# Kernel tuning notes

Measured on AMD Instinct MI355X. Metric: run time of the kernel, lower is better.

## Reference

```python
import jax, jax.numpy as jnp
import numpy as np
import math

D = 256; NH = 8; NG = 64; META = 6

def _linear(x, w, b):
    return x @ w.T + b

def setup_inputs():
    key = jax.random.key(0)
    ks = jax.random.split(key, 12)
    B, T, TG = 32, 4096, 1024
    def rn(k, shape, s=0.02):
        return jax.random.normal(k, shape, dtype=jnp.float32) * s
    q = jax.random.normal(ks[0], (1, NG, D), dtype=jnp.float32)
    q = q / jnp.clip(jnp.linalg.norm(q, axis=-1, keepdims=True), 1e-6)
    # fibonacci unit sphere anchor, scaled by 0.4
    idx = jnp.arange(NG, dtype=jnp.float32)
    golden = (1.0 + math.sqrt(5.0)) / 2.0
    theta = 2.0 * math.pi * idx / golden
    z = jnp.clip(1.0 - (2.0 * idx + 1.0) / NG, -1.0 + 1e-6, 1.0 - 1e-6)
    r = jnp.sqrt(jnp.clip(1.0 - z * z, 0.0))
    pts = jnp.stack([r * jnp.cos(theta), r * jnp.sin(theta), z], axis=-1)
    pts = pts / jnp.clip(jnp.linalg.norm(pts, axis=-1, keepdims=True), 1e-6)
    p0 = (pts * 0.4)[None]
    ph_b2 = jnp.array([0.0] * 6 + [-2.0] * 4, dtype=jnp.float32)
    return dict(
        local_feat=jax.random.normal(ks[1], (B, D, T), dtype=jnp.float32),
        global_feat=jax.random.normal(ks[2], (B, D, TG), dtype=jnp.float32),
        meta=jax.random.uniform(ks[3], (B, META), dtype=jnp.float32),
        queries=q, p0_anchor=p0,
        in_proj_w=rn(ks[4], (3 * D, D)), in_proj_b=jnp.zeros((3 * D,), jnp.float32),
        out_proj_w=rn(ks[5], (D, D)), out_proj_b=jnp.zeros((D,), jnp.float32),
        ln_g=jnp.ones((D,), jnp.float32), ln_b=jnp.zeros((D,), jnp.float32),
        meta_w=rn(ks[6], (D, META)), meta_b=jnp.zeros((D,), jnp.float32),
        temporal_w=rn(ks[7], (D, D)), temporal_b=jnp.zeros((D,), jnp.float32),
        shift_w=rn(ks[8], (3, D)), shift_b=jnp.zeros((3,), jnp.float32),
        ph_w1=rn(ks[9], (D // 2, D)), ph_b1=jnp.zeros((D // 2,), jnp.float32),
        ph_w2=rn(ks[10], (10, D // 2)), ph_b2=ph_b2,
        wave_delay_scale=jnp.float32(0.1),
        envelope_bias=jnp.float32(0.5),
    )

def reference(local_feat, global_feat, meta, queries, p0_anchor, in_proj_w, in_proj_b,
              out_proj_w, out_proj_b, ln_g, ln_b, meta_w, meta_b, temporal_w, temporal_b,
              shift_w, shift_b, ph_w1, ph_b1, ph_w2, ph_b2, wave_delay_scale, envelope_bias):
    B, _, T = local_feat.shape
    DH = D // NH
    kv = jnp.transpose(global_feat, (0, 2, 1))                        # [B,TG,D]
    q = jnp.broadcast_to(queries, (B, NG, D))
    wq, wk, wv = in_proj_w[:D], in_proj_w[D:2 * D], in_proj_w[2 * D:]
    bq, bk, bv = in_proj_b[:D], in_proj_b[D:2 * D], in_proj_b[2 * D:]
    qh = _linear(q, wq, bq).reshape(B, NG, NH, DH)
    kh = _linear(kv, wk, bk).reshape(B, -1, NH, DH)
    vh = _linear(kv, wv, bv).reshape(B, -1, NH, DH)
    attn = jax.nn.softmax(jnp.einsum('bqhd,bkhd->bhqk', qh, kh) / math.sqrt(DH), axis=-1)
    ctx = jnp.einsum('bhqk,bkhd->bqhd', attn, vh).reshape(B, NG, D)
    x = q + _linear(ctx, out_proj_w, out_proj_b)
    mu = x.mean(-1, keepdims=True)
    var = ((x - mu) ** 2).mean(-1, keepdims=True)
    q_static = (x - mu) / jnp.sqrt(var + 1e-5) * ln_g + ln_b
    q_static = q_static + jax.nn.gelu(_linear(meta, meta_w, meta_b), approximate=False)[:, None, :]
    params = _linear(jax.nn.gelu(_linear(q_static, ph_w1, ph_b1), approximate=False), ph_w2, ph_b2)
    p0_delta = jnp.tanh(params[..., 0:3]) * 0.2
    heart_shift = jnp.tanh(_linear(global_feat.mean(-1), shift_w, shift_b)) * 0.3
    p_pos = p0_anchor + p0_delta + heart_shift[:, None, :]            # [B,NG,3]
    dnorm = jnp.clip(jnp.linalg.norm(params[..., 3:6], axis=-1, keepdims=True), 1e-6)
    dipole_dir = params[..., 3:6] / dnorm
    volume_xyz = jax.nn.sigmoid(params[..., 6:9]) * 0.5 + 0.001
    amplitude = jax.nn.sigmoid(params[..., 9]) + 1e-4                 # [B,NG]
    tw = _linear(q_static, temporal_w, temporal_b)                    # [B,NG,D]
    temporal_logits = jnp.einsum('bnc,bct->bnt', tw, local_feat) / math.sqrt(D)
    idx_sa = jnp.argmax(amplitude, axis=1)                            # [B]
    p_sa = jnp.take_along_axis(p_pos, idx_sa[:, None, None], axis=1)  # [B,1,3]
    dist = jnp.linalg.norm(p_pos - p_sa, axis=-1)                     # [B,NG]
    delay = jnp.clip(jax.nn.softplus(wave_delay_scale) * dist, 0.0, 0.1)
    base_x = jnp.linspace(-1.0, 1.0, T)
    grid_x = base_x[None, None, :] - delay[..., None]                 # [B,NG,T]
    # grid_sample(bilinear, zeros, align_corners=True): grid_y hits rows exactly,
    # so it reduces to 1D linear interp along time with zero padding.
    x_pix = (grid_x + 1.0) * 0.5 * (T - 1)
    x0 = jnp.floor(x_pix).astype(jnp.int32)
    x1 = x0 + 1
    w1 = x_pix - x0.astype(x_pix.dtype)
    w0 = 1.0 - w1
    def samp(xi):
        g = jnp.take_along_axis(temporal_logits, jnp.clip(xi, 0, T - 1), axis=-1)
        return g * ((xi >= 0) & (xi <= T - 1)).astype(g.dtype)
    shifted = w0 * samp(x0) + w1 * samp(x1)
    envelope_t = jax.nn.sigmoid(shifted + envelope_bias)              # [B,NG,T]
    return amplitude, p_pos, dipole_dir, volume_xyz, envelope_t
```

## Files before the change

### kernel.cpp

```cpp
#include <hip/hip_runtime.h>
#include <hip/hip_bf16.h>
#include <math.h>

typedef __hip_bfloat16 bf16;
typedef short s16x8 __attribute__((ext_vector_type(8)));
typedef float f32x4 __attribute__((ext_vector_type(4)));

#define NDIM 256
#define NTG 1024
#define NT 4096

__device__ __forceinline__ float gelu_exact(float x) {
    return 0.5f * x * (1.0f + erff(x * 0.70710678118654752440f));
}
__device__ __forceinline__ float sigmoidf_(float x) {
    return 1.0f / (1.0f + __expf(-x));
}
__device__ __forceinline__ short f2bf_s(float x) {
    union { bf16 h; short s; } cv;
    cv.h = __float2bfloat16(x);
    return cv.s;
}
__device__ __forceinline__ float bf2f(short s) {
    union { bf16 h; short s; } cv;
    cv.s = s;
    return __bfloat162float(cv.h);
}

__global__ __launch_bounds__(256) void k_prep(
        const float* __restrict__ ipw, const float* __restrict__ opw,
        const float* __restrict__ twm, const float* __restrict__ pw1,
        const float* __restrict__ queries, const float* __restrict__ ipb,
        float* __restrict__ opwT, float* __restrict__ twT, float* __restrict__ pw1T,
        bf16* __restrict__ wkvK, bf16* __restrict__ wkvV,
        float* __restrict__ qh, float* __restrict__ gmean) {
    int blk = blockIdx.x, tid = threadIdx.x;
    if (blk < 384) {
        int id = blk * 256 + tid;
        if (id < 65536) {
            int k = id >> 8, c = id & 255;
            opwT[id] = opw[c * 256 + k];
            twT[id]  = twm[c * 256 + k];
        } else {
            int id2 = id - 65536;
            int k = id2 >> 7, m = id2 & 127;
            pw1T[id2] = pw1[m * 256 + k];
        }
    } else if (blk < 640) {
        int id = (blk - 384) * 256 + tid;
        wkvK[id] = __float2bfloat16(ipw[65536 + id]);
        wkvV[id] = __float2bfloat16(ipw[131072 + id]);
    } else if (blk < 704) {
        __shared__ float qrow[256];
        int n = blk - 640, c = tid;
        qrow[c] = queries[n * 256 + c];
        __syncthreads();
        float s = ipb[c];
        const float* wr = ipw + c * 256;
        for (int k = 0; k < 256; ++k) s += qrow[k] * wr[k];
        qh[n * 256 + c] = s;
    } else {
        gmean[(blk - 704) * 256 + tid] = 0.f;
    }
}

__global__ __launch_bounds__(256) void k_gft(const float* __restrict__ gf,
                                             bf16* __restrict__ gfT,
                                             float* __restrict__ gmean) {
    __shared__ float tile[64][65];
    int tid = threadIdx.x;
    int t0 = blockIdx.x * 64, c0 = blockIdx.y * 64, b = blockIdx.z;
    int tt = tid & 63, ci = tid >> 6;
    #pragma unroll
    for (int r = 0; r < 16; ++r) {
        int cl = ci * 16 + r;
        tile[cl][tt] = gf[((size_t)(b * 256 + c0 + cl)) * NTG + t0 + tt];
    }
    __syncthreads();
    int cc = tid & 63, ti = tid >> 6;
    #pragma unroll
    for (int r = 0; r < 16; ++r) {
        int tl = ti * 16 + r;
        gfT[((size_t)(b * 1024 + t0 + tl)) * 256 + c0 + cc] =
            __float2bfloat16(tile[cc][tl]);
    }
    float ps = 0.f;
    #pragma unroll
    for (int r = 0; r < 16; ++r) ps += tile[cc][ti * 16 + r];
    atomicAdd(&gmean[b * 256 + c0 + cc], ps * (1.0f / 1024.0f));
}

__global__ void k_metahs(const float* __restrict__ meta, const float* __restrict__ mw,
                         const float* __restrict__ mb, const float* __restrict__ gmean,
                         const float* __restrict__ sw, const float* __restrict__ sb,
                         float* __restrict__ metag, float* __restrict__ hshift) {
    int b = blockIdx.x, c = threadIdx.x;
    float s = mb[c];
    #pragma unroll
    for (int j = 0; j < 6; ++j) s += meta[b * 6 + j] * mw[c * 6 + j];
    metag[b * 256 + c] = gelu_exact(s);
    if (c < 3) {
        float t = sb[c];
        const float* gm = gmean + b * 256;
        for (int k = 0; k < 256; ++k) t += gm[k] * sw[c * 256 + k];
        hshift[b * 4 + c] = tanhf(t) * 0.3f;
    }
}

__global__ __launch_bounds__(256) void k_kv(
        const short* __restrict__ gfT, const short* __restrict__ wkvK,
        const short* __restrict__ wkvV, const float* __restrict__ ipb,
        short* __restrict__ kvh, short* __restrict__ vTg) {
    int tid = threadIdx.x;
    int w = tid >> 6, lane = tid & 63, lm = lane & 15, quad = lane >> 4;
    int t0 = blockIdx.x * 128 + w * 32;
    int sel = blockIdx.y >> 2;
    int n0 = (blockIdx.y & 3) * 64;
    int b = blockIdx.z;
    if (sel == 0) {
        f32x4 acc[4][2];
        #pragma unroll
        for (int ni = 0; ni < 4; ++ni)
            #pragma unroll
            for (int mt = 0; mt < 2; ++mt) acc[ni][mt] = (f32x4)(0.0f);
        #pragma unroll
        for (int ks = 0; ks < 8; ++ks) {
            int c = ks * 32 + quad * 8;
            s16x8 bg[2];
            #pragma unroll
            for (int mt = 0; mt < 2; ++mt)
                bg[mt] = *(const s16x8*)&gfT[((size_t)(b * 1024 + t0 + mt * 16 + lm)) * 256 + c];
            #pragma unroll
            for (int ni = 0; ni < 4; ++ni) {
                s16x8 aw = *(const s16x8*)&wkvK[(n0 + ni * 16 + lm) * 256 + c];
                #pragma unroll
                for (int mt = 0; mt < 2; ++mt)
                    acc[ni][mt] = __builtin_amdgcn_mfma_f32_16x16x32_bf16(aw, bg[mt], acc[ni][mt], 0, 0, 0);
            }
        }
        #pragma unroll
        for (int ni = 0; ni < 4; ++ni) {
            int nb4 = n0 + ni * 16 + quad * 4;
            float4 bias = *(const float4*)&ipb[256 + nb4];
            #pragma unroll
            for (int mt = 0; mt < 2; ++mt) {
                int t = t0 + mt * 16 + lm;
                ushort4 o;
                o.x = (unsigned short)f2bf_s(acc[ni][mt][0] + bias.x);
                o.y = (unsigned short)f2bf_s(acc[ni][mt][1] + bias.y);
                o.z = (unsigned short)f2bf_s(acc[ni][mt][2] + bias.z);
                o.w = (unsigned short)f2bf_s(acc[ni][mt][3] + bias.w);
                *(ushort4*)&kvh[((size_t)(b * 1024 + t)) * 256 + nb4] = o;
            }
        }
    } else {
        f32x4 acc[2][4];
        #pragma unroll
        for (int mt = 0; mt < 2; ++mt)
            #pragma unroll
            for (int ni = 0; ni < 4; ++ni) acc[mt][ni] = (f32x4)(0.0f);
        #pragma unroll
        for (int ks = 0; ks < 8; ++ks) {
            int c = ks * 32 + quad * 8;
            s16x8 ag[2];
            #pragma unroll
            for (int mt = 0; mt < 2; ++mt)
                ag[mt] = *(const s16x8*)&gfT[((size_t)(b * 1024 + t0 + mt * 16 + lm)) * 256 + c];
            #pragma unroll
            for (int ni = 0; ni < 4; ++ni) {
                s16x8 bw = *(const s16x8*)&wkvV[(n0 + ni * 16 + lm) * 256 + c];
                #pragma unroll
                for (int mt = 0; mt < 2; ++mt)
                    acc[mt][ni] = __builtin_amdgcn_mfma_f32_16x16x32_bf16(ag[mt], bw, acc[mt][ni], 0, 0, 0);
            }
        }
        #pragma unroll
        for (int ni = 0; ni < 4; ++ni) {
            int nv = n0 + ni * 16 + lm;
            float bias = ipb[512 + nv];
            #pragma unroll
            for (int mt = 0; mt < 2; ++mt) {
                int t4 = t0 + mt * 16 + quad * 4;
                ushort4 o;
                o.x = (unsigned short)f2bf_s(acc[mt][ni][0] + bias);
                o.y = (unsigned short)f2bf_s(acc[mt][ni][1] + bias);
                o.z = (unsigned short)f2bf_s(acc[mt][ni][2] + bias);
                o.w = (unsigned short)f2bf_s(acc[mt][ni][3] + bias);
                *(ushort4*)&vTg[((size_t)(b * 256 + nv)) * 1024 + t4] = o;
            }
        }
    }
}

__global__ __launch_bounds__(256) void k_attn(
        const short* __restrict__ kvh, const short* __restrict__ vTg,
        const float* __restrict__ qh,
        float* __restrict__ o_half, float* __restrict__ l_half) {
    __shared__ short pT[4][64 * 40];
    __shared__ float obuf[4][64 * 36];
    __shared__ float lbuf[4 * 64];
    int tid = threadIdx.x;
    int w = tid >> 6, lane = tid & 63, lm = lane & 15, quad = lane >> 4;
    int half = blockIdx.x, h = blockIdx.y, b = blockIdx.z;
    s16x8 aq[4];
    #pragma unroll
    for (int mt = 0; mt < 4; ++mt) {
        const float* qp = qh + (mt * 16 + lm) * 256 + h * 32 + quad * 8;
        #pragma unroll
        for (int j = 0; j < 8; ++j) aq[mt][j] = f2bf_s(qp[j]);
    }
    f32x4 acco[2][4];
    #pragma unroll
    for (int dt = 0; dt < 2; ++dt)
        #pragma unroll
        for (int qt = 0; qt < 4; ++qt) acco[dt][qt] = (f32x4)(0.0f);
    float lp[4][4];
    #pragma unroll
    for (int mt = 0; mt < 4; ++mt)
        #pragma unroll
        for (int r = 0; r < 4; ++r) lp[mt][r] = 0.f;
    const float scale = 0.17677669529663687f;
    int kb = half * 512 + w * 128;
    for (int ch = 0; ch < 4; ++ch) {
        int n0 = kb + ch * 32;
        #pragma unroll
        for (int nt = 0; nt < 2; ++nt) {
            int key = n0 + nt * 16 + lm;
            s16x8 bk = *(const s16x8*)&kvh[((size_t)(b * 1024 + key)) * 256 + h * 32 + quad * 8];
            f32x4 zero = {0.f, 0.f, 0.f, 0.f};
            #pragma unroll
            for (int mt = 0; mt < 4; ++mt) {
                f32x4 S = __builtin_amdgcn_mfma_f32_16x16x32_bf16(aq[mt], bk, zero, 0, 0, 0);
                #pragma unroll
                for (int r = 0; r < 4; ++r) {
                    float e = __expf(S[r] * scale);
                    lp[mt][r] += e;
                    pT[w][(mt * 16 + quad * 4 + r) * 40 + nt * 16 + lm] = f2bf_s(e);
                }
            }
        }
        s16x8 av[2], bp[4];
        #pragma unroll
        for (int dt = 0; dt < 2; ++dt)
            av[dt] = *(const s16x8*)&vTg[((size_t)(b * 256 + h * 32 + dt * 16 + lm)) * 1024 + n0 + quad * 8];
        #pragma unroll
        for (int qt = 0; qt < 4; ++qt)
            bp[qt] = *(const s16x8*)&pT[w][(qt * 16 + lm) * 40 + quad * 8];
        #pragma unroll
        for (int dt = 0; dt < 2; ++dt)
            #pragma unroll
            for (int qt = 0; qt < 4; ++qt)
                acco[dt][qt] = __builtin_amdgcn_mfma_f32_16x16x32_bf16(av[dt], bp[qt], acco[dt][qt], 0, 0, 0);
    }
    #pragma unroll
    for (int mt = 0; mt < 4; ++mt)
        #pragma unroll
        for (int r = 0; r < 4; ++r) {
            float v = lp[mt][r];
            v += __shfl_xor(v, 1); v += __shfl_xor(v, 2);
            v += __shfl_xor(v, 4); v += __shfl_xor(v, 8);
            lp[mt][r] = v;
        }
    #pragma unroll
    for (int dt = 0; dt < 2; ++dt)
        #pragma unroll
        for (int qt = 0; qt < 4; ++qt) {
            int q = qt * 16 + lm;
            float4 t;
            t.x = acco[dt][qt][0]; t.y = acco[dt][qt][1];
            t.z = acco[dt][qt][2]; t.w = acco[dt][qt][3];
            *(float4*)&obuf[w][q * 36 + dt * 16 + quad * 4] = t;
        }
    if (lm == 0) {
        #pragma unroll
        for (int mt = 0; mt < 4; ++mt)
            #pragma unroll
            for (int r = 0; r < 4; ++r)
                lbuf[w * 64 + mt * 16 + quad * 4 + r] = lp[mt][r];
    }
    __syncthreads();
    int q = tid & 63, dg = tid >> 6;
    int blk = (b * 8 + h) * 2 + half;
    float l = lbuf[q] + lbuf[64 + q] + lbuf[128 + q] + lbuf[192 + q];
    float o[8];
    #pragma unroll
    for (int j = 0; j < 8; ++j) o[j] = 0.f;
    #pragma unroll
    for (int w2 = 0; w2 < 4; ++w2) {
        const float* src = &obuf[w2][q * 36 + dg * 8];
        #pragma unroll
        for (int j = 0; j < 8; ++j) o[j] += src[j];
    }
    float* dst = &o_half[(((size_t)blk * 64) + q) * 32 + dg * 8];
    #pragma unroll
    for (int j = 0; j < 8; ++j) dst[j] = o[j];
    if (dg == 0) l_half[blk * 64 + q] = l;
}

__global__ __launch_bounds__(256) void k_post(
        const float* __restrict__ o_half, const float* __restrict__ l_half,
        const float* __restrict__ queries,
        const float* __restrict__ opwT, const float* __restrict__ opb,
        const float* __restrict__ lng, const float* __restrict__ lnb,
        const float* __restrict__ metag, const float* __restrict__ hshift,
        const float* __restrict__ twT, const float* __restrict__ tbv,
        const float* __restrict__ pw1T, const float* __restrict__ pb1,
        const float* __restrict__ pw2, const float* __restrict__ pb2,
        const float* __restrict__ p0a,
        bf16* __restrict__ twbf, float* __restrict__ out_amp,
        float* __restrict__ out_ppos, float* __restrict__ out_dip,
        float* __restrict__ out_vol) {
    __shared__ float cs[8][256];
    __shared__ float xs[8][256];
    __shared__ float qs[8][256];
    __shared__ float h1[8][128];
    __shared__ float ps[8][10];
    int tid = threadIdx.x;
    int n0 = blockIdx.x * 8, b = blockIdx.y;
    {
        int h = tid >> 5, d = tid & 31;
        int blk0 = (b * 8 + h) * 2;
        #pragma unroll
        for (int r = 0; r < 8; ++r) {
            int q = n0 + r;
            float l = l_half[blk0 * 64 + q] + l_half[(blk0 + 1) * 64 + q];
            float v0 = o_half[(((size_t)blk0 * 64) + q) * 32 + d];
            float v1 = o_half[(((size_t)(blk0 + 1) * 64) + q) * 32 + d];
            cs[r][tid] = (v0 + v1) / l;
        }
    }
    __syncthreads();
    {
        int c = tid;
        float a[8];
        #pragma unroll
        for (int nn = 0; nn < 8; ++nn) a[nn] = opb[c];
        for (int k = 0; k < 256; ++k) {
            float w = opwT[k * 256 + c];
            #pragma unroll
            for (int nn = 0; nn < 8; ++nn) a[nn] += cs[nn][k] * w;
        }
        #pragma unroll
        for (int nn = 0; nn < 8; ++nn)
            xs[nn][c] = queries[(n0 + nn) * 256 + c] + a[nn];
    }
    __syncthreads();
    {
        int w = tid >> 6, lane = tid & 63;
        for (int i = 0; i < 2; ++i) {
            int nr = w + i * 4;
            float x0 = xs[nr][lane], x1 = xs[nr][lane + 64],
                  x2 = xs[nr][lane + 128], x3 = xs[nr][lane + 192];
            float s = x0 + x1 + x2 + x3;
            #pragma unroll
            for (int off = 32; off >= 1; off >>= 1) s += __shfl_xor(s, off);
            float mu = s * (1.0f / 256.0f);
            float e0 = x0 - mu, e1 = x1 - mu, e2 = x2 - mu, e3 = x3 - mu;
            float v = e0*e0 + e1*e1 + e2*e2 + e3*e3;
            #pragma unroll
            for (int off = 32; off >= 1; off >>= 1) v += __shfl_xor(v, off);
            float rstd = 1.0f / sqrtf(v * (1.0f / 256.0f) + 1e-5f);
            #pragma unroll
            for (int j = 0; j < 4; ++j) {
                int c = lane + 64 * j;
                qs[nr][c] = (xs[nr][c] - mu) * rstd * lng[c] + lnb[c] + metag[b * 256 + c];
            }
        }
    }
    __syncthreads();
    {
        int c = tid;
        float a[8];
        #pragma unroll
        for (int nn = 0; nn < 8; ++nn) a[nn] = tbv[c];
        for (int k = 0; k < 256; ++k) {
            float w = twT[k * 256 + c];
            #pragma unroll
            for (int nn = 0; nn < 8; ++nn) a[nn] += qs[nn][k] * w;
        }
        #pragma unroll
        for (int nn = 0; nn < 8; ++nn)
            twbf[(size_t)(b * 64 + n0 + nn) * 256 + c] = __float2bfloat16(a[nn]);
    }
    {
        int m = tid & 127, g = tid >> 7;
        float a[4];
        #pragma unroll
        for (int q4 = 0; q4 < 4; ++q4) a[q4] = pb1[m];
        for (int k = 0; k < 256; ++k) {
            float w = pw1T[k * 128 + m];
            #pragma unroll
            for (int q4 = 0; q4 < 4; ++q4) a[q4] += qs[g * 4 + q4][k] * w;
        }
        #pragma unroll
        for (int q4 = 0; q4 < 4; ++q4) h1[g * 4 + q4][m] = gelu_exact(a[q4]);
    }
    __syncthreads();
    if (tid < 80) {
        int nr = tid / 10, j = tid % 10;
        float s = pb2[j];
        for (int m = 0; m < 128; ++m) s += h1[nr][m] * pw2[j * 128 + m];
        ps[nr][j] = s;
    }
    __syncthreads();
    if (tid < 8) {
        int nr = tid;
        int gn = b * 64 + n0 + nr;
        #pragma unroll
        for (int j = 0; j < 3; ++j) {
            float delta = tanhf(ps[nr][j]) * 0.2f;
            out_ppos[gn * 3 + j] = p0a[(n0 + nr) * 3 + j] + delta + hshift[b * 4 + j];
        }
        float d0 = ps[nr][3], d1 = ps[nr][4], d2 = ps[nr][5];
        float dn = fmaxf(sqrtf(d0 * d0 + d1 * d1 + d2 * d2), 1e-6f);
        out_dip[gn * 3 + 0] = d0 / dn;
        out_dip[gn * 3 + 1] = d1 / dn;
        out_dip[gn * 3 + 2] = d2 / dn;
        #pragma unroll
        for (int j = 0; j < 3; ++j)
            out_vol[gn * 3 + j] = sigmoidf_(ps[nr][6 + j]) * 0.5f + 0.001f;
        out_amp[gn] = sigmoidf_(ps[nr][9]) + 0.0001f;
    }
}

__global__ __launch_bounds__(256) void k_temporal(
        const float* __restrict__ lf, const short* __restrict__ twbf,
        short* __restrict__ logits) {
    __shared__ __align__(16) short tws[64 * 264];
    __shared__ __align__(16) short lfs[32 * 132];
    int tid = threadIdx.x;
    int t0 = blockIdx.x * 128, b = blockIdx.y;
    int wave = tid >> 6, lane = tid & 63;
    int lm = lane & 15, quad = lane >> 4;

    #pragma unroll
    for (int i = 0; i < 8; ++i) {
        int id = i * 256 + tid;
        int n = id >> 5, c8 = id & 31;
        s16x8 v = *(const s16x8*)&twbf[(size_t)(b * 64 + n) * 256 + c8 * 8];
        *(s16x8*)&tws[n * 264 + c8 * 8] = v;
    }

    f32x4 acc[2][4];
    #pragma unroll
    for (int mi = 0; mi < 2; ++mi)
        #pragma unroll
        for (int ni = 0; ni < 4; ++ni) acc[mi][ni] = (f32x4)(0.0f);

    for (int ksi = 0; ksi < 8; ++ksi) {
        int c0 = ksi * 32;
        #pragma unroll
        for (int r = 0; r < 4; ++r) {
            int id = r * 256 + tid;
            int c = id >> 5, t4 = id & 31;
            float4 f = *(const float4*)&lf[((size_t)(b * 256 + c0 + c)) * 4096 + t0 + t4 * 4];
            ushort4 o;
            o.x = (unsigned short)f2bf_s(f.x);
            o.y = (unsigned short)f2bf_s(f.y);
            o.z = (unsigned short)f2bf_s(f.z);
            o.w = (unsigned short)f2bf_s(f.w);
            *(ushort4*)&lfs[c * 132 + t4 * 4] = o;
        }
        __syncthreads();
        #pragma unroll
        for (int mi = 0; mi < 2; ++mi) {
            int tl = wave * 32 + mi * 16 + lm;
            s16x8 af;
            #pragma unroll
            for (int j = 0; j < 8; ++j)
                af[j] = lfs[(quad * 8 + j) * 132 + tl];
            #pragma unroll
            for (int ni = 0; ni < 4; ++ni) {
                s16x8 bfr = *(const s16x8*)&tws[(ni * 16 + lm) * 264 + c0 + quad * 8];
                acc[mi][ni] = __builtin_amdgcn_mfma_f32_16x16x32_bf16(af, bfr, acc[mi][ni], 0, 0, 0);
            }
        }
        __syncthreads();
    }
    #pragma unroll
    for (int mi = 0; mi < 2; ++mi) {
        #pragma unroll
        for (int ni = 0; ni < 4; ++ni) {
            int n = ni * 16 + lm;
            int t = t0 + wave * 32 + mi * 16 + quad * 4;
            ushort4 o;
            o.x = (unsigned short)f2bf_s(acc[mi][ni][0] * 0.0625f);
            o.y = (unsigned short)f2bf_s(acc[mi][ni][1] * 0.0625f);
            o.z = (unsigned short)f2bf_s(acc[mi][ni][2] * 0.0625f);
            o.w = (unsigned short)f2bf_s(acc[mi][ni][3] * 0.0625f);
            *(ushort4*)&logits[(size_t)(b * 64 + n) * 4096 + t] = o;
        }
    }
}

__global__ void k_envelope(const short* __restrict__ logits,
                           const float* __restrict__ out_amp,
                           const float* __restrict__ out_ppos,
                           const float* __restrict__ wds,
                           const float* __restrict__ ebp,
                           float* __restrict__ env) {
    int blk = blockIdx.x;
    int bn = blk >> 2, seg = blk & 3;
    int b = bn >> 6, n = bn & 63;
    int tid = threadIdx.x;
    int lane = tid & 63;
    float v = out_amp[b * 64 + lane];
    int idx = lane;
    #pragma unroll
    for (int off = 1; off < 64; off <<= 1) {
        float ov = __shfl_xor(v, off);
        int oi = __shfl_xor(idx, off);
        if (ov > v || (ov == v && oi < idx)) { v = ov; idx = oi; }
    }
    float dx = out_ppos[(b * 64 + n) * 3 + 0] - out_ppos[(b * 64 + idx) * 3 + 0];
    float dy = out_ppos[(b * 64 + n) * 3 + 1] - out_ppos[(b * 64 + idx) * 3 + 1];
    float dz = out_ppos[(b * 64 + n) * 3 + 2] - out_ppos[(b * 64 + idx) * 3 + 2];
    float dist = sqrtf(dx * dx + dy * dy + dz * dz);
    float sp = log1pf(expf(wds[0]));
    float dl = fminf(fmaxf(sp * dist, 0.f), 0.1f);
    float eb = ebp[0];
    const short* gl = logits + (size_t)bn * 4096;
    int t_base = seg * 1024 + tid * 4;
    float ov4[4];
    #pragma unroll
    for (int u = 0; u < 4; ++u) {
        int t = t_base + u;
        float xb = fmaf((float)t, 2.0f / 4095.0f, -1.0f);
        float xp = (xb - dl + 1.0f) * 2047.5f;
        float x0f = floorf(xp);
        int x0 = (int)x0f;
        float w1 = xp - x0f, w0 = 1.0f - w1;
        float g0 = (x0 >= 0 && x0 <= 4095) ? bf2f(gl[x0]) : 0.f;
        int x1 = x0 + 1;
        float g1 = (x1 >= 0 && x1 <= 4095) ? bf2f(gl[x1]) : 0.f;
        float sh = w0 * g0 + w1 * g1;
        ov4[u] = 1.0f / (1.0f + __expf(-(sh + eb)));
    }
    float4 o; o.x = ov4[0]; o.y = ov4[1]; o.z = ov4[2]; o.w = ov4[3];
    *reinterpret_cast<float4*>(&env[(size_t)bn * 4096 + t_base]) = o;
}

extern "C" void kernel_launch(void* const* d_in, const int* in_sizes, int n_in,
                              void* d_out, int out_size, void* d_ws, size_t ws_size,
                              hipStream_t stream) {
    const float* lf   = (const float*)d_in[0];
    const float* gf   = (const float*)d_in[1];
    const float* meta = (const float*)d_in[2];
    const float* qrs  = (const float*)d_in[3];
    const float* p0a  = (const float*)d_in[4];
    const float* ipw  = (const float*)d_in[5];
    const float* ipb  = (const float*)d_in[6];
    const float* opw  = (const float*)d_in[7];
    const float* opb  = (const float*)d_in[8];
    const float* lng  = (const float*)d_in[9];
    const float* lnb  = (const float*)d_in[10];
    const float* mw   = (const float*)d_in[11];
    const float* mb   = (const float*)d_in[12];
    const float* twm  = (const float*)d_in[13];
    const float* tbv  = (const float*)d_in[14];
    const float* sw   = (const float*)d_in[15];
    const float* sb   = (const float*)d_in[16];
    const float* pw1  = (const float*)d_in[17];
    const float* pb1  = (const float*)d_in[18];
    const float* pw2  = (const float*)d_in[19];
    const float* pb2  = (const float*)d_in[20];
    const float* wds  = (const float*)d_in[21];
    const float* ebp  = (const float*)d_in[22];

    char* ws = (char*)d_ws;
    short* kvh    = (short*)(ws);
    short* vTg    = (short*)(ws + 16777216);
    short* gfT    = (short*)(ws + 33554432);
    short* logits = (short*)(ws + 50331648);
    float* o_half = (float*)(ws + 67108864);
    float* l_half = (float*)(ws + 71303168);
    short* twbf   = (short*)(ws + 71434240);
    float* qh     = (float*)(ws + 72482816);
    float* gmean  = (float*)(ws + 72548352);
    float* metag  = (float*)(ws + 72581120);
    float* hshift = (float*)(ws + 72613888);
    float* opwT   = (float*)(ws + 72614400);
    float* twT    = (float*)(ws + 72876544);
    float* pw1T   = (float*)(ws + 73138688);
    short* wkvK   = (short*)(ws + 73269760);
    short* wkvV   = (short*)(ws + 73400832);

    float* out_amp  = (float*)d_out;
    float* out_ppos = out_amp + 2048;
    float* out_dip  = out_amp + 8192;
    float* out_vol  = out_amp + 14336;
    float* env      = out_amp + 20480;

    k_prep<<<712, 256, 0, stream>>>(ipw, opw, twm, pw1, qrs, ipb,
                                    opwT, twT, pw1T, (bf16*)wkvK, (bf16*)wkvV,
                                    qh, gmean);
    k_gft<<<dim3(16, 4, 32), 256, 0, stream>>>(gf, (bf16*)gfT, gmean);
    k_metahs<<<32, 256, 0, stream>>>(meta, mw, mb, gmean, sw, sb, metag, hshift);
    k_kv<<<dim3(8, 8, 32), 256, 0, stream>>>(gfT, wkvK, wkvV, ipb, kvh, vTg);
    k_attn<<<dim3(2, 8, 32), 256, 0, stream>>>(kvh, vTg, qh, o_half, l_half);
    k_post<<<dim3(8, 32), 256, 0, stream>>>(o_half, l_half, qrs, opwT, opb, lng, lnb,
                                            metag, hshift, twT, tbv, pw1T, pb1, pw2, pb2,
                                            p0a, (bf16*)twbf, out_amp, out_ppos,
                                            out_dip, out_vol);
    k_temporal<<<dim3(32, 32), 256, 0, stream>>>(lf, twbf, logits);
    k_envelope<<<8192, 256, 0, stream>>>(logits, out_amp, out_ppos, wds, ebp, env);
}
```

Baseline: 422.8 us.

## Fuse prep kernels, double-buffer temporal GEMM loads, halve post rows per block

The global-feature transpose moves into k_prep, and its atomic mean is replaced by per-tile partial sums. Those partials are reduced inside extra blocks of k_kv, which also compute the meta and shift values, so two launches disappear. k_temporal now prefetches the next channel slab into registers and double-buffers it in LDS, overlapping global loads with MFMA work and dropping one barrier per step. k_post handles 4 queries per block instead of 8, doubling the block count to improve parallelism at the cost of reloading the weights more often.

```diff
diff --git a/kernel.cpp b/kernel.cpp
--- a/kernel.cpp
+++ b/kernel.cpp
@@ -28,95 +28,108 @@
 }
 
 __global__ __launch_bounds__(256) void k_prep(
-        const float* __restrict__ ipw, const float* __restrict__ opw,
-        const float* __restrict__ twm, const float* __restrict__ pw1,
-        const float* __restrict__ queries, const float* __restrict__ ipb,
+        const float* __restrict__ gf, const float* __restrict__ ipw,
+        const float* __restrict__ opw, const float* __restrict__ twm,
+        const float* __restrict__ pw1, const float* __restrict__ queries,
+        const float* __restrict__ ipb,
+        bf16* __restrict__ gfT, float* __restrict__ partial,
         float* __restrict__ opwT, float* __restrict__ twT, float* __restrict__ pw1T,
         bf16* __restrict__ wkvK, bf16* __restrict__ wkvV,
-        float* __restrict__ qh, float* __restrict__ gmean) {
+        float* __restrict__ qh) {
+    __shared__ float smem[64 * 65 + 256];
     int blk = blockIdx.x, tid = threadIdx.x;
-    if (blk < 384) {
-        int id = blk * 256 + tid;
-        if (id < 65536) {
-            int k = id >> 8, c = id & 255;
-            opwT[id] = opw[c * 256 + k];
-            twT[id]  = twm[c * 256 + k];
+    if (blk < 2048) {
+        float (*tile)[65] = (float(*)[65])smem;
+        float* psum = smem + 64 * 65;
+        int t0 = (blk & 15) * 64, c0 = ((blk >> 4) & 3) * 64, b = blk >> 6;
+        int tt = tid & 63, ci = tid >> 6;
+        #pragma unroll
+        for (int r = 0; r < 16; ++r) {
+            int cl = ci * 16 + r;
+            tile[cl][tt] = gf[((size_t)(b * 256 + c0 + cl)) * NTG + t0 + tt];
+        }
+        __syncthreads();
+        int cc = tid & 63, ti = tid >> 6;
+        #pragma unroll
+        for (int r = 0; r < 16; ++r) {
+            int tl = ti * 16 + r;
+            gfT[((size_t)(b * 1024 + t0 + tl)) * 256 + c0 + cc] =
+                __float2bfloat16(tile[cc][tl]);
+        }
+        float ps = 0.f;
+        #pragma unroll
+        for (int r = 0; r < 16; ++r) ps += tile[cc][ti * 16 + r];
+        psum[tid] = ps;
+        __syncthreads();
+        if (tid < 64) {
+            float s = psum[tid] + psum[tid + 64] + psum[tid + 128] + psum[tid + 192];
+            partial[(b * 256 + c0 + tid) * 16 + (blk & 15)] = s;
+        }
+    } else {
+        int pblk = blk - 2048;
+        if (pblk < 384) {
+            int id = pblk * 256 + tid;
+            if (id < 65536) {
+                int k = id >> 8, c = id & 255;
+                opwT[id] = opw[c * 256 + k];
+                twT[id]  = twm[c * 256 + k];
+            } else {
+                int id2 = id - 65536;
+                int k = id2 >> 7, m = id2 & 127;
+                pw1T[id2] = pw1[m * 256 + k];
+            }
+        } else if (pblk < 640) {
+            int id = (pblk - 384) * 256 + tid;
+            wkvK[id] = __float2bfloat16(ipw[65536 + id]);
+            wkvV[id] = __float2bfloat16(ipw[131072 + id]);
         } else {
-            int id2 = id - 65536;
-            int k = id2 >> 7, m = id2 & 127;
-            pw1T[id2] = pw1[m * 256 + k];
-        }
-    } else if (blk < 640) {
-        int id = (blk - 384) * 256 + tid;
-        wkvK[id] = __float2bfloat16(ipw[65536 + id]);
-        wkvV[id] = __float2bfloat16(ipw[131072 + id]);
-    } else if (blk < 704) {
-        __shared__ float qrow[256];
-        int n = blk - 640, c = tid;
-        qrow[c] = queries[n * 256 + c];
-        __syncthreads();
-        float s = ipb[c];
-        const float* wr = ipw + c * 256;
-        for (int k = 0; k < 256; ++k) s += qrow[k] * wr[k];
-        qh[n * 256 + c] = s;
-    } else {
-        gmean[(blk - 704) * 256 + tid] = 0.f;
-    }
-}
-
-__global__ __launch_bounds__(256) void k_gft(const float* __restrict__ gf,
-                                             bf16* __restrict__ gfT,
-                                             float* __restrict__ gmean) {
-    __shared__ float tile[64][65];
-    int tid = threadIdx.x;
-    int t0 = blockIdx.x * 64, c0 = blockIdx.y * 64, b = blockIdx.z;
-    int tt = tid & 63, ci = tid >> 6;
-    #pragma unroll
-    for (int r = 0; r < 16; ++r) {
-        int cl = ci * 16 + r;
-        tile[cl][tt] = gf[((size_t)(b * 256 + c0 + cl)) * NTG + t0 + tt];
-    }
-    __syncthreads();
-    int cc = tid & 63, ti = tid >> 6;
-    #pragma unroll
-    for (int r = 0; r < 16; ++r) {
-        int tl = ti * 16 + r;
-        gfT[((size_t)(b * 1024 + t0 + tl)) * 256 + c0 + cc] =
-            __float2bfloat16(tile[cc][tl]);
-    }
-    float ps = 0.f;
-    #pragma unroll
-    for (int r = 0; r < 16; ++r) ps += tile[cc][ti * 16 + r];
-    atomicAdd(&gmean[b * 256 + c0 + cc], ps * (1.0f / 1024.0f));
-}
-
-__global__ void k_metahs(const float* __restrict__ meta, const float* __restrict__ mw,
-                         const float* __restrict__ mb, const float* __restrict__ gmean,
-                         const float* __restrict__ sw, const float* __restrict__ sb,
-                         float* __restrict__ metag, float* __restrict__ hshift) {
-    int b = blockIdx.x, c = threadIdx.x;
-    float s = mb[c];
-    #pragma unroll
-    for (int j = 0; j < 6; ++j) s += meta[b * 6 + j] * mw[c * 6 + j];
-    metag[b * 256 + c] = gelu_exact(s);
-    if (c < 3) {
-        float t = sb[c];
-        const float* gm = gmean + b * 256;
-        for (int k = 0; k < 256; ++k) t += gm[k] * sw[c * 256 + k];
-        hshift[b * 4 + c] = tanhf(t) * 0.3f;
+            float* qrow = smem;
+            int n = pblk - 640, c = tid;
+            qrow[c] = queries[n * 256 + c];
+            __syncthreads();
+            float s = ipb[c];
+            const float* wr = ipw + c * 256;
+            for (int k = 0; k < 256; ++k) s += qrow[k] * wr[k];
+            qh[n * 256 + c] = s;
+        }
     }
 }
 
 __global__ __launch_bounds__(256) void k_kv(
         const short* __restrict__ gfT, const short* __restrict__ wkvK,
         const short* __restrict__ wkvV, const float* __restrict__ ipb,
-        short* __restrict__ kvh, short* __restrict__ vTg) {
+        const float* __restrict__ meta, const float* __restrict__ mw,
+        const float* __restrict__ mb, const float* __restrict__ partial,
+        const float* __restrict__ sw, const float* __restrict__ sb,
+        short* __restrict__ kvh, short* __restrict__ vTg,
+        float* __restrict__ metag, float* __restrict__ hshift) {
+    int blk = blockIdx.x;
     int tid = threadIdx.x;
+    if (blk >= 2048) {
+        __shared__ float gm[256];
+        int b = blk - 2048, c = tid;
+        float m = 0.f;
+        const float* pp = partial + (b * 256 + c) * 16;
+        #pragma unroll
+        for (int tt = 0; tt < 16; ++tt) m += pp[tt];
+        gm[c] = m * (1.0f / 1024.0f);
+        float s = mb[c];
+        #pragma unroll
+        for (int j = 0; j < 6; ++j) s += meta[b * 6 + j] * mw[c * 6 + j];
+        metag[b * 256 + c] = gelu_exact(s);
+        __syncthreads();
+        if (c < 3) {
+            float t = sb[c];
+            for (int k = 0; k < 256; ++k) t += gm[k] * sw[c * 256 + k];
+            hshift[b * 4 + c] = tanhf(t) * 0.3f;
+        }
+        return;
+    }
     int w = tid >> 6, lane = tid & 63, lm = lane & 15, quad = lane >> 4;
-    int t0 = blockIdx.x * 128 + w * 32;
-    int sel = blockIdx.y >> 2;
-    int n0 = (blockIdx.y & 3) * 64;
-    int b = blockIdx.z;
+    int bx = blk & 7, byq = (blk >> 3) & 7, b = blk >> 6;
+    int t0 = bx * 128 + w * 32;
+    int sel = byq >> 2;
+    int n0 = (byq & 3) * 64;
     if (sel == 0) {
         f32x4 acc[4][2];
         #pragma unroll
@@ -310,18 +323,18 @@
         bf16* __restrict__ twbf, float* __restrict__ out_amp,
         float* __restrict__ out_ppos, float* __restrict__ out_dip,
         float* __restrict__ out_vol) {
-    __shared__ float cs[8][256];
-    __shared__ float xs[8][256];
-    __shared__ float qs[8][256];
-    __shared__ float h1[8][128];
-    __shared__ float ps[8][10];
+    __shared__ float cs[4][256];
+    __shared__ float xs[4][256];
+    __shared__ float qs[4][256];
+    __shared__ float h1[4][128];
+    __shared__ float ps[4][10];
     int tid = threadIdx.x;
-    int n0 = blockIdx.x * 8, b = blockIdx.y;
+    int n0 = blockIdx.x * 4, b = blockIdx.y;
     {
         int h = tid >> 5, d = tid & 31;
         int blk0 = (b * 8 + h) * 2;
         #pragma unroll
-        for (int r = 0; r < 8; ++r) {
+        for (int r = 0; r < 4; ++r) {
             int q = n0 + r;
             float l = l_half[blk0 * 64 + q] + l_half[(blk0 + 1) * 64 + q];
             float v0 = o_half[(((size_t)blk0 * 64) + q) * 32 + d];
@@ -332,78 +345,76 @@
     __syncthreads();
     {
         int c = tid;
-        float a[8];
-        #pragma unroll
-        for (int nn = 0; nn < 8; ++nn) a[nn] = opb[c];
+        float a[4];
+        #pragma unroll
+        for (int nn = 0; nn < 4; ++nn) a[nn] = opb[c];
         for (int k = 0; k < 256; ++k) {
             float w = opwT[k * 256 + c];
             #pragma unroll
-            for (int nn = 0; nn < 8; ++nn) a[nn] += cs[nn][k] * w;
-        }
-        #pragma unroll
-        for (int nn = 0; nn < 8; ++nn)
+            for (int nn = 0; nn < 4; ++nn) a[nn] += cs[nn][k] * w;
+        }
+        #pragma unroll
+        for (int nn = 0; nn < 4; ++nn)
             xs[nn][c] = queries[(n0 + nn) * 256 + c] + a[nn];
     }
     __syncthreads();
     {
         int w = tid >> 6, lane = tid & 63;
-        for (int i = 0; i < 2; ++i) {
-            int nr = w + i * 4;
-            float x0 = xs[nr][lane], x1 = xs[nr][lane + 64],
-                  x2 = xs[nr][lane + 128], x3 = xs[nr][lane + 192];
-            float s = x0 + x1 + x2 + x3;
-            #pragma unroll
-            for (int off = 32; off >= 1; off >>= 1) s += __shfl_xor(s, off);
-            float mu = s * (1.0f / 256.0f);
-            float e0 = x0 - mu, e1 = x1 - mu, e2 = x2 - mu, e3 = x3 - mu;
-            float v = e0*e0 + e1*e1 + e2*e2 + e3*e3;
-            #pragma unroll
-            for (int off = 32; off >= 1; off >>= 1) v += __shfl_xor(v, off);
-            float rstd = 1.0f / sqrtf(v * (1.0f / 256.0f) + 1e-5f);
-            #pragma unroll
-            for (int j = 0; j < 4; ++j) {
-                int c = lane + 64 * j;
-                qs[nr][c] = (xs[nr][c] - mu) * rstd * lng[c] + lnb[c] + metag[b * 256 + c];
-            }
+        int nr = w;
+        float x0 = xs[nr][lane], x1 = xs[nr][lane + 64],
+              x2 = xs[nr][lane + 128], x3 = xs[nr][lane + 192];
+        float s = x0 + x1 + x2 + x3;
+        #pragma unroll
+        for (int off = 32; off >= 1; off >>= 1) s += __shfl_xor(s, off);
+        float mu = s * (1.0f / 256.0f);
+        float e0 = x0 - mu, e1 = x1 - mu, e2 = x2 - mu, e3 = x3 - mu;
+        float v = e0*e0 + e1*e1 + e2*e2 + e3*e3;
+        #pragma unroll
+        for (int off = 32; off >= 1; off >>= 1) v += __shfl_xor(v, off);
+        float rstd = 1.0f / sqrtf(v * (1.0f / 256.0f) + 1e-5f);
+        #pragma unroll
+        for (int j = 0; j < 4; ++j) {
+            int c = lane + 64 * j;
+            qs[nr][c] = (xs[nr][c] - mu) * rstd * lng[c] + lnb[c] + metag[b * 256 + c];
         }
     }
     __syncthreads();
     {
         int c = tid;
-        float a[8];
-        #pragma unroll
-        for (int nn = 0; nn < 8; ++nn) a[nn] = tbv[c];
+        float a[4];
+        #pragma unroll
+        for (int nn = 0; nn < 4; ++nn) a[nn] = tbv[c];
         for (int k = 0; k < 256; ++k) {
             float w = twT[k * 256 + c];
             #pragma unroll
-            for (int nn = 0; nn < 8; ++nn) a[nn] += qs[nn][k] * w;
-        }
-        #pragma unroll
-        for (int nn = 0; nn < 8; ++nn)
+            for (int nn = 0; nn < 4; ++nn) a[nn] += qs[nn][k] * w;
+        }
+        #pragma unroll
+        for (int nn = 0; nn < 4; ++nn)
             twbf[(size_t)(b * 64 + n0 + nn) * 256 + c] = __float2bfloat16(a[nn]);
     }
     {
         int m = tid & 127, g = tid >> 7;
-        float a[4];
-        #pragma unroll
-        for (int q4 = 0; q4 < 4; ++q4) a[q4] = pb1[m];
+        float a[2];
+        #pragma unroll
+        for (int q2 = 0; q2 < 2; ++q2) a[q2] = pb1[m];
         for (int k = 0; k < 256; ++k) {
             float w = pw1T[k * 128 + m];
             #pragma unroll
-            for (int q4 = 0; q4 < 4; ++q4) a[q4] += qs[g * 4 + q4][k] * w;
-        }
-        #pragma unroll
-        for (int q4 = 0; q4 < 4; ++q4) h1[g * 4 + q4][m] = gelu_exact(a[q4]);
+            for (int q2 = 0; q2 < 2; ++q2) a[q2] += qs[g * 2 + q2][k] * w;
+        }
+        #pragma unroll
+        for (int q2 = 0; q2 < 2; ++q2) h1[g * 2 + q2][m] = gelu_exact(a[q2]);
     }
     __syncthreads();
-    if (tid < 80) {
+    if (tid < 40) {
         int nr = tid / 10, j = tid % 10;
         float s = pb2[j];
         for (int m = 0; m < 128; ++m) s += h1[nr][m] * pw2[j * 128 + m];
         ps[nr][j] = s;
     }
     __syncthreads();
-    if (tid < 8) {
+    if (tid < 4) {
         int nr = tid;
         int gn = b * 64 + n0 + nr;
         #pragma unroll
@@ -427,7 +438,7 @@
         const float* __restrict__ lf, const short* __restrict__ twbf,
         short* __restrict__ logits) {
     __shared__ __align__(16) short tws[64 * 264];
-    __shared__ __align__(16) short lfs[32 * 132];
+    __shared__ __align__(16) short lfs[2][32 * 132];
     int tid = threadIdx.x;
     int t0 = blockIdx.x * 128, b = blockIdx.y;
     int wave = tid >> 6, lane = tid & 63;
@@ -441,38 +452,69 @@
         *(s16x8*)&tws[n * 264 + c8 * 8] = v;
     }
 
+    float4 fr[4];
+    #pragma unroll
+    for (int r = 0; r < 4; ++r) {
+        int id = r * 256 + tid;
+        int c = id >> 5, t4 = id & 31;
+        fr[r] = *(const float4*)&lf[((size_t)(b * 256 + c)) * 4096 + t0 + t4 * 4];
+    }
+    #pragma unroll
+    for (int r = 0; r < 4; ++r) {
+        int id = r * 256 + tid;
+        int c = id >> 5, t4 = id & 31;
+        ushort4 o;
+        o.x = (unsigned short)f2bf_s(fr[r].x);
+        o.y = (unsigned short)f2bf_s(fr[r].y);
+        o.z = (unsigned short)f2bf_s(fr[r].z);
+        o.w = (unsigned short)f2bf_s(fr[r].w);
+        *(ushort4*)&lfs[0][c * 132 + t4 * 4] = o;
+    }
+
     f32x4 acc[2][4];
     #pragma unroll
     for (int mi = 0; mi < 2; ++mi)
         #pragma unroll
         for (int ni = 0; ni < 4; ++ni) acc[mi][ni] = (f32x4)(0.0f);
 
+    __syncthreads();
+
     for (int ksi = 0; ksi < 8; ++ksi) {
+        int cur = ksi & 1;
+        if (ksi < 7) {
+            int c0n = (ksi + 1) * 32;
+            #pragma unroll
+            for (int r = 0; r < 4; ++r) {
+                int id = r * 256 + tid;
+                int c = id >> 5, t4 = id & 31;
+                fr[r] = *(const float4*)&lf[((size_t)(b * 256 + c0n + c)) * 4096 + t0 + t4 * 4];
+            }
+        }
         int c0 = ksi * 32;
-        #pragma unroll
-        for (int r = 0; r < 4; ++r) {
-            int id = r * 256 + tid;
-            int c = id >> 5, t4 = id & 31;
-            float4 f = *(const float4*)&lf[((size_t)(b * 256 + c0 + c)) * 4096 + t0 + t4 * 4];
-            ushort4 o;
-            o.x = (unsigned short)f2bf_s(f.x);
-            o.y = (unsigned short)f2bf_s(f.y);
-            o.z = (unsigned short)f2bf_s(f.z);
-            o.w = (unsigned short)f2bf_s(f.w);
-            *(ushort4*)&lfs[c * 132 + t4 * 4] = o;
-        }
-        __syncthreads();
         #pragma unroll
         for (int mi = 0; mi < 2; ++mi) {
             int tl = wave * 32 + mi * 16 + lm;
             s16x8 af;
             #pragma unroll
             for (int j = 0; j < 8; ++j)
-                af[j] = lfs[(quad * 8 + j) * 132 + tl];
+                af[j] = lfs[cur][(quad * 8 + j) * 132 + tl];
             #pragma unroll
             for (int ni = 0; ni < 4; ++ni) {
                 s16x8 bfr = *(const s16x8*)&tws[(ni * 16 + lm) * 264 + c0 + quad * 8];
                 acc[mi][ni] = __builtin_amdgcn_mfma_f32_16x16x32_bf16(af, bfr, acc[mi][ni], 0, 0, 0);
+            }
+        }
+        if (ksi < 7) {
+            #pragma unroll
+            for (int r = 0; r < 4; ++r) {
+                int id = r * 256 + tid;
+                int c = id >> 5, t4 = id & 31;
+                ushort4 o;
+                o.x = (unsigned short)f2bf_s(fr[r].x);
+                o.y = (unsigned short)f2bf_s(fr[r].y);
+                o.z = (unsigned short)f2bf_s(fr[r].z);
+                o.w = (unsigned short)f2bf_s(fr[r].w);
+                *(ushort4*)&lfs[cur ^ 1][c * 132 + t4 * 4] = o;
             }
         }
         __syncthreads();
@@ -576,7 +618,6 @@
     float* l_half = (float*)(ws + 71303168);
     short* twbf   = (short*)(ws + 71434240);
     float* qh     = (float*)(ws + 72482816);
-    float* gmean  = (float*)(ws + 72548352);
     float* metag  = (float*)(ws + 72581120);
     float* hshift = (float*)(ws + 72613888);
     float* opwT   = (float*)(ws + 72614400);
@@ -584,6 +625,7 @@
     float* pw1T   = (float*)(ws + 73138688);
     short* wkvK   = (short*)(ws + 73269760);
     short* wkvV   = (short*)(ws + 73400832);
+    float* partial= (float*)(ws + 73531904);
 
     float* out_amp  = (float*)d_out;
     float* out_ppos = out_amp + 2048;
@@ -591,17 +633,16 @@
     float* out_vol  = out_amp + 14336;
     float* env      = out_amp + 20480;
 
-    k_prep<<<712, 256, 0, stream>>>(ipw, opw, twm, pw1, qrs, ipb,
-                                    opwT, twT, pw1T, (bf16*)wkvK, (bf16*)wkvV,
-                                    qh, gmean);
-    k_gft<<<dim3(16, 4, 32), 256, 0, stream>>>(gf, (bf16*)gfT, gmean);
-    k_metahs<<<32, 256, 0, stream>>>(meta, mw, mb, gmean, sw, sb, metag, hshift);
-    k_kv<<<dim3(8, 8, 32), 256, 0, stream>>>(gfT, wkvK, wkvV, ipb, kvh, vTg);
+    k_prep<<<2752, 256, 0, stream>>>(gf, ipw, opw, twm, pw1, qrs, ipb,
+                                     (bf16*)gfT, partial, opwT, twT, pw1T,
+                                     (bf16*)wkvK, (bf16*)wkvV, qh);
+    k_kv<<<2080, 256, 0, stream>>>(gfT, wkvK, wkvV, ipb, meta, mw, mb, partial,
+                                   sw, sb, kvh, vTg, metag, hshift);
     k_attn<<<dim3(2, 8, 32), 256, 0, stream>>>(kvh, vTg, qh, o_half, l_half);
-    k_post<<<dim3(8, 32), 256, 0, stream>>>(o_half, l_half, qrs, opwT, opb, lng, lnb,
-                                            metag, hshift, twT, tbv, pw1T, pb1, pw2, pb2,
-                                            p0a, (bf16*)twbf, out_amp, out_ppos,
-                                            out_dip, out_vol);
+    k_post<<<dim3(16, 32), 256, 0, stream>>>(o_half, l_half, qrs, opwT, opb, lng, lnb,
+                                             metag, hshift, twT, tbv, pw1T, pb1, pw2, pb2,
+                                             p0a, (bf16*)twbf, out_amp, out_ppos,
+                                             out_dip, out_vol);
     k_temporal<<<dim3(32, 32), 256, 0, stream>>>(lf, twbf, logits);
     k_envelope<<<8192, 256, 0, stream>>>(logits, out_amp, out_ppos, wds, ebp, env);
 }
```

Result: faster. 401.8 us (-4.9%).
